# Kernel tuning notes

Measured on AMD Instinct MI355X. Metric: run time of the kernel, lower is better.

Reference implementation:

```python
import jax, jax.numpy as jnp
import numpy as np

B, N = 128, 196
HDIM, VDIM, ATT = 512, 2048, 512


def setup_inputs() -> dict:
    key = jax.random.key(0)
    ks = jax.random.split(key, 8)
    s_w = 1.0 / np.sqrt(HDIM)
    s_u = 1.0 / np.sqrt(VDIM)
    s_v = 1.0 / np.sqrt(ATT)
    return {
        "h": jax.random.normal(ks[0], (B, HDIM), dtype=jnp.float32),
        "V": jax.random.normal(ks[1], (B, N, VDIM), dtype=jnp.float32),
        "Ww": jax.random.uniform(ks[2], (HDIM, ATT), jnp.float32, -s_w, s_w),
        "Wb": jax.random.uniform(ks[3], (ATT,), jnp.float32, -s_w, s_w),
        "Uw": jax.random.uniform(ks[4], (VDIM, ATT), jnp.float32, -s_u, s_u),
        "Ub": jax.random.uniform(ks[5], (ATT,), jnp.float32, -s_u, s_u),
        "vw": jax.random.uniform(ks[6], (ATT, 1), jnp.float32, -s_v, s_v),
        "vb": jax.random.uniform(ks[7], (1,), jnp.float32, -s_v, s_v),
    }


def reference(h, V, Ww, Wb, Uw, Ub, vw, vb):
    # W(h): [B, A]; U(V): [B, N, A]
    wh = h @ Ww + Wb
    uv = jnp.einsum("bnv,va->bna", V, Uw) + Ub
    # e: [B, N, 1] scores via v(tanh(...))
    e = jnp.tanh(wh[:, None, :] + uv) @ vw + vb
    a = jax.nn.softmax(e, axis=1)          # softmax over N locations
    ctx = jnp.sum(a * V, axis=1)            # [B, vdim]
    return ctx, a.squeeze(-1)
```

## Files before the change

### kernel.cpp

```cpp
#include <hip/hip_runtime.h>
#include <hip/hip_bf16.h>

#define B_    128
#define N_    196
#define HDIM  512
#define VDIM  2048
#define ATT   512
#define M_TOT (B_ * N_)

#define BM  128
#define BKK 64
#define BN  128
#define NT  (VDIM / BKK)

typedef float  f32x4  __attribute__((ext_vector_type(4)));
typedef __bf16 bf16x8 __attribute__((ext_vector_type(8)));

__device__ __forceinline__ void gload_lds16(const void* g, void* l) {
    __builtin_amdgcn_global_load_lds(
        (const __attribute__((address_space(1))) void*)g,
        (__attribute__((address_space(3))) void*)l, 16, 0, 0);
}

__device__ __forceinline__ float fast_tanh(float x) {
    float ax = fabsf(x);
    float e  = __expf(-2.f * ax);
    float t  = (1.f - e) / (1.f + e);
    return copysignf(t, x);
}

__global__ void k_conv(const float* __restrict__ V, __bf16* __restrict__ Vb, int n8) {
    int idx    = blockIdx.x * blockDim.x + threadIdx.x;
    int stride = gridDim.x * blockDim.x;
    for (int i = idx; i < n8; i += stride) {
        const float4* s = reinterpret_cast<const float4*>(V + (size_t)i * 8);
        float4 x = s[0], y = s[1];
        bf16x8 w;
        w[0] = (__bf16)x.x; w[1] = (__bf16)x.y; w[2] = (__bf16)x.z; w[3] = (__bf16)x.w;
        w[4] = (__bf16)y.x; w[5] = (__bf16)y.y; w[6] = (__bf16)y.z; w[7] = (__bf16)y.w;
        reinterpret_cast<bf16x8*>(Vb)[i] = w;
    }
}

__global__ void k_transpose(const float* __restrict__ Uw, __bf16* __restrict__ UwT) {
    __shared__ __bf16 st[64][65];
    int k0 = blockIdx.x * 64;
    int c0 = blockIdx.y * 64;
    int t  = threadIdx.x;
#pragma unroll
    for (int i = 0; i < 16; ++i) {
        int lin = i * 256 + t;
        int kk = lin >> 6, cc = lin & 63;
        st[kk][cc] = (__bf16)Uw[(size_t)(k0 + kk) * ATT + c0 + cc];
    }
    __syncthreads();
#pragma unroll
    for (int i = 0; i < 16; ++i) {
        int lin = i * 256 + t;
        int cc = lin >> 6, kk = lin & 63;
        UwT[(size_t)(c0 + cc) * VDIM + k0 + kk] = st[kk][cc];
    }
}

__global__ void k_wh(const float* __restrict__ h, const float* __restrict__ Ww,
                     const float* __restrict__ Wb, const float* __restrict__ Ub,
                     float* __restrict__ whp) {
    __shared__ float hs[HDIM];
    int b = blockIdx.x;
    int t = threadIdx.x;
    hs[t]       = h[(size_t)b * HDIM + t];
    hs[t + 256] = h[(size_t)b * HDIM + t + 256];
    __syncthreads();
    float acc0 = 0.f, acc1 = 0.f;
    for (int k = 0; k < HDIM; ++k) {
        float hv = hs[k];
        acc0 += hv * Ww[(size_t)k * ATT + t];
        acc1 += hv * Ww[(size_t)k * ATT + t + 256];
    }
    whp[(size_t)b * ATT + t]       = acc0 + Wb[t] + Ub[t];
    whp[(size_t)b * ATT + t + 256] = acc1 + Wb[t + 256] + Ub[t + 256];
}

template <bool PRECONV>
__global__ __launch_bounds__(256, 2) void k_scores(
    const float* __restrict__ Vf, const __bf16* __restrict__ Vb,
    const __bf16* __restrict__ UwT, const float* __restrict__ whp,
    const float* __restrict__ vw, float* __restrict__ e_part)
{
    __shared__ __align__(16) __bf16 As[2][BM][BKK];
    __shared__ __align__(16) __bf16 Bs[2][BN][BKK];
    __shared__ float red[2][BM];

    int bid = blockIdx.x;
    int lid = (bid & 7) * (784 / 8) + (bid >> 3);
    int mtile = lid >> 2;
    int cc    = lid & 3;
    int m0 = mtile * BM;
    int c0 = cc * BN;
    int t    = threadIdx.x;
    int lane = t & 63;
    int wave = t >> 6;
    int wr = wave >> 1;
    int wc = wave & 1;

    f32x4 acc[4][4];
#pragma unroll
    for (int i = 0; i < 4; ++i)
#pragma unroll
        for (int j = 0; j < 4; ++j) acc[i][j] = (f32x4){0.f, 0.f, 0.f, 0.f};

    int lr  = lane >> 3;
    int csw = ((lane & 7) ^ (lr & 7)) * 8;
    const __bf16* AgS = PRECONV ? (Vb + (size_t)(m0 + wave * 32 + lr) * VDIM + csw) : nullptr;
    const __bf16* BgS = UwT + (size_t)(c0 + wave * 32 + lr) * VDIM + csw;
    __bf16* Al0 = &As[0][wave * 32 + lr][(lane & 7) * 8];
    __bf16* Bl0 = &Bs[0][wave * 32 + lr][(lane & 7) * 8];

    int ra = t >> 1;
    int ka = (t & 1) * 32;
    const float* Af = PRECONV ? nullptr : (Vf + (size_t)(m0 + ra) * VDIM + ka);

    int lcol = lane & 15;
    int lg4  = lane >> 4;

#define STAGE(buf, kt)                                                          \
    do {                                                                        \
        int kk0 = (kt) * BKK;                                                   \
        if (PRECONV) {                                                          \
            _Pragma("unroll")                                                   \
            for (int i = 0; i < 4; ++i) {                                       \
                gload_lds16(AgS + kk0 + (size_t)i * 8 * VDIM,                   \
                            Al0 + (buf) * (BM * BKK) + i * 8 * BKK);            \
                gload_lds16(BgS + kk0 + (size_t)i * 8 * VDIM,                   \
                            Bl0 + (buf) * (BN * BKK) + i * 8 * BKK);            \
            }                                                                   \
        } else {                                                                \
            _Pragma("unroll")                                                   \
            for (int i = 0; i < 4; ++i)                                         \
                gload_lds16(BgS + kk0 + (size_t)i * 8 * VDIM,                   \
                            Bl0 + (buf) * (BN * BKK) + i * 8 * BKK);            \
            const float4* src = reinterpret_cast<const float4*>(Af + kk0);      \
            _Pragma("unroll")                                                   \
            for (int i = 0; i < 4; ++i) {                                       \
                float4 x = src[2 * i];                                          \
                float4 y = src[2 * i + 1];                                      \
                bf16x8 w;                                                       \
                w[0] = (__bf16)x.x; w[1] = (__bf16)x.y;                         \
                w[2] = (__bf16)x.z; w[3] = (__bf16)x.w;                         \
                w[4] = (__bf16)y.x; w[5] = (__bf16)y.y;                         \
                w[6] = (__bf16)y.z; w[7] = (__bf16)y.w;                         \
                int ch = (((t & 1) * 4 + i) ^ (ra & 7)) * 8;                    \
                *reinterpret_cast<bf16x8*>(&As[buf][ra][ch]) = w;               \
            }                                                                   \
        }                                                                       \
    } while (0)

    int arow_base = wr * 64;
    int bcol_base = wc * 64;

    STAGE(0, 0);
    __syncthreads();

    for (int kt = 0; kt < NT; ++kt) {
        int buf = kt & 1;
        if (kt + 1 < NT) STAGE(buf ^ 1, kt + 1);

#pragma unroll
        for (int ks = 0; ks < 2; ++ks) {
            bf16x8 af[4], bfr[4];
#pragma unroll
            for (int i = 0; i < 4; ++i) {
                int row = arow_base + i * 16 + lcol;
                int ch  = ((ks * 4 + lg4) ^ (row & 7)) * 8;
                af[i] = *reinterpret_cast<const bf16x8*>(&As[buf][row][ch]);
            }
#pragma unroll
            for (int j = 0; j < 4; ++j) {
                int row = bcol_base + j * 16 + lcol;
                int ch  = ((ks * 4 + lg4) ^ (row & 7)) * 8;
                bfr[j] = *reinterpret_cast<const bf16x8*>(&Bs[buf][row][ch]);
            }
            __builtin_amdgcn_s_setprio(1);
#pragma unroll
            for (int i = 0; i < 4; ++i)
#pragma unroll
                for (int j = 0; j < 4; ++j)
                    acc[i][j] = __builtin_amdgcn_mfma_f32_16x16x32_bf16(af[i], bfr[j], acc[i][j], 0, 0, 0);
            __builtin_amdgcn_s_setprio(0);
        }
        __syncthreads();
    }
#undef STAGE

    int lrow4 = lg4 * 4;
    float rowsum[4][4];
#pragma unroll
    for (int i = 0; i < 4; ++i)
#pragma unroll
        for (int r = 0; r < 4; ++r) rowsum[i][r] = 0.f;

#pragma unroll
    for (int j = 0; j < 4; ++j) {
        int col = c0 + wc * 64 + j * 16 + lcol;
        float vwv = vw[col];
#pragma unroll
        for (int i = 0; i < 4; ++i) {
#pragma unroll
            for (int r = 0; r < 4; ++r) {
                int m = m0 + wr * 64 + i * 16 + lrow4 + r;
                int b = m / N_;
                float x = acc[i][j][r] + whp[(size_t)b * ATT + col];
                rowsum[i][r] += fast_tanh(x) * vwv;
            }
        }
    }
#pragma unroll
    for (int i = 0; i < 4; ++i) {
#pragma unroll
        for (int r = 0; r < 4; ++r) {
            float v = rowsum[i][r];
            v += __shfl_xor(v, 1);
            v += __shfl_xor(v, 2);
            v += __shfl_xor(v, 4);
            v += __shfl_xor(v, 8);
            if (lcol == 0)
                red[wc][wr * 64 + i * 16 + lrow4 + r] = v;
        }
    }
    __syncthreads();
    if (t < BM)
        e_part[(size_t)cc * M_TOT + m0 + t] = red[0][t] + red[1][t];
}

__global__ void k_softmax(const float* __restrict__ e_part, const float* __restrict__ vb,
                          float* __restrict__ a_out) {
    int b = blockIdx.x;
    int t = threadIdx.x;
    __shared__ float sm[256];
    float ev = 0.f;
    float e  = -1e30f;
    if (t < N_) {
        int m = b * N_ + t;
        ev = e_part[m] + e_part[M_TOT + m] + e_part[2 * M_TOT + m] + e_part[3 * M_TOT + m] + vb[0];
        e = ev;
    }
    sm[t] = e;
    __syncthreads();
    for (int s = 128; s > 0; s >>= 1) {
        if (t < s) sm[t] = fmaxf(sm[t], sm[t + s]);
        __syncthreads();
    }
    float mx = sm[0];
    __syncthreads();
    float ex = (t < N_) ? __expf(ev - mx) : 0.f;
    sm[t] = ex;
    __syncthreads();
    for (int s = 128; s > 0; s >>= 1) {
        if (t < s) sm[t] += sm[t + s];
        __syncthreads();
    }
    float inv = 1.f / sm[0];
    if (t < N_) a_out[(size_t)b * N_ + t] = ex * inv;
}

__global__ void k_ctx_bf(const __bf16* __restrict__ Vb, const float* __restrict__ a,
                         float* __restrict__ ctx) {
    int b  = blockIdx.x;
    int ch = blockIdx.y;
    int t  = threadIdx.x;
    __shared__ float as_[N_];
    for (int i = t; i < N_; i += 128) as_[i] = a[(size_t)b * N_ + i];
    __syncthreads();
    int col = ch * 1024 + t * 8;
    const __bf16* Vp = Vb + (size_t)b * N_ * VDIM + col;
    float av[8] = {0.f, 0.f, 0.f, 0.f, 0.f, 0.f, 0.f, 0.f};
    for (int n = 0; n < N_; ++n) {
        bf16x8 v = *reinterpret_cast<const bf16x8*>(Vp + (size_t)n * VDIM);
        float an = as_[n];
#pragma unroll
        for (int j = 0; j < 8; ++j) av[j] += an * (float)v[j];
    }
    f32x4 lo = {av[0], av[1], av[2], av[3]};
    f32x4 hi = {av[4], av[5], av[6], av[7]};
    f32x4* dst = reinterpret_cast<f32x4*>(ctx + (size_t)b * VDIM + col);
    dst[0] = lo;
    dst[1] = hi;
}

__global__ void k_ctx_f32(const float* __restrict__ V, const float* __restrict__ a,
                          float* __restrict__ ctx) {
    int b  = blockIdx.x;
    int ch = blockIdx.y;
    int t  = threadIdx.x;
    __shared__ float as_[N_];
    for (int i = t; i < N_; i += 128) as_[i] = a[(size_t)b * N_ + i];
    __syncthreads();
    int col = ch * 512 + t * 4;
    const f32x4* Vp = reinterpret_cast<const f32x4*>(V + (size_t)b * N_ * VDIM + col);
    f32x4 accv = {0.f, 0.f, 0.f, 0.f};
    for (int n = 0; n < N_; ++n)
        accv += as_[n] * Vp[(size_t)n * (VDIM / 4)];
    *reinterpret_cast<f32x4*>(ctx + (size_t)b * VDIM + col) = accv;
}

extern "C" void kernel_launch(void* const* d_in, const int* in_sizes, int n_in,
                              void* d_out, int out_size, void* d_ws, size_t ws_size,
                              hipStream_t stream) {
    const float* h  = (const float*)d_in[0];
    const float* V  = (const float*)d_in[1];
    const float* Ww = (const float*)d_in[2];
    const float* Wb = (const float*)d_in[3];
    const float* Uw = (const float*)d_in[4];
    const float* Ub = (const float*)d_in[5];
    const float* vw = (const float*)d_in[6];
    const float* vb = (const float*)d_in[7];

    float* out     = (float*)d_out;
    float* ctx_out = out;
    float* a_out   = out + (size_t)B_ * VDIM;

    const size_t vb_bytes = (size_t)B_ * N_ * VDIM * sizeof(__bf16);
    const size_t tail     = 2u * 1024 * 1024 + 256 * 1024 + (size_t)4 * M_TOT * 4 + 4096;
    bool preconv = ws_size >= vb_bytes + tail;

    char*   ws   = (char*)d_ws;
    __bf16* Vb   = (__bf16*)ws;
    char*   rest = ws + (preconv ? vb_bytes : 0);
    __bf16* UwT   = (__bf16*)rest;
    float*  whp   = (float*)(rest + 2u * 1024 * 1024);
    float*  e_prt = (float*)(rest + 2u * 1024 * 1024 + 256 * 1024);

    if (preconv) {
        int n8 = (B_ * N_ * VDIM) / 8;
        k_conv<<<2048, 256, 0, stream>>>(V, Vb, n8);
    }
    k_transpose<<<dim3(VDIM / 64, ATT / 64), 256, 0, stream>>>(Uw, UwT);
    k_wh<<<dim3(B_), 256, 0, stream>>>(h, Ww, Wb, Ub, whp);
    if (preconv)
        k_scores<true><<<dim3((M_TOT / BM) * (ATT / BN)), 256, 0, stream>>>(V, Vb, UwT, whp, vw, e_prt);
    else
        k_scores<false><<<dim3((M_TOT / BM) * (ATT / BN)), 256, 0, stream>>>(V, Vb, UwT, whp, vw, e_prt);
    k_softmax<<<dim3(B_), 256, 0, stream>>>(e_prt, vb, a_out);
    if (preconv)
        k_ctx_bf<<<dim3(B_, 2), 128, 0, stream>>>(Vb, a_out, ctx_out);
    else
        k_ctx_f32<<<dim3(B_, 4), 128, 0, stream>>>(V, a_out, ctx_out);
}
```

Baseline: 177.8 us.

## Fuse V bf16 conversion into scores GEMM and merge prep kernels

Removes the separate fp32-to-bf16 conversion pass over V: the scores GEMM now loads fp32 V tiles into registers, converts them and writes them to padded LDS (stride 72 instead of an XOR swizzle). The column-tile-0 blocks also write the bf16 copy of V to global memory for the later context kernel. Prefetch of the next A tile into registers is overlapped with the MFMA work, and the transpose and W(h) kernels are merged into one launch. The aim is to avoid one full read and write of V and some launch overhead, at the cost of each GEMM block reading fp32 A four times (once per column tile) and higher register pressure.

```diff
diff --git a/kernel.cpp b/kernel.cpp
--- a/kernel.cpp
+++ b/kernel.cpp
@@ -12,6 +12,7 @@
 #define BKK 64
 #define BN  128
 #define NT  (VDIM / BKK)
+#define LDA 72
 
 typedef float  f32x4  __attribute__((ext_vector_type(4)));
 typedef __bf16 bf16x8 __attribute__((ext_vector_type(8)));
@@ -29,65 +30,52 @@
     return copysignf(t, x);
 }
 
-__global__ void k_conv(const float* __restrict__ V, __bf16* __restrict__ Vb, int n8) {
-    int idx    = blockIdx.x * blockDim.x + threadIdx.x;
-    int stride = gridDim.x * blockDim.x;
-    for (int i = idx; i < n8; i += stride) {
-        const float4* s = reinterpret_cast<const float4*>(V + (size_t)i * 8);
-        float4 x = s[0], y = s[1];
-        bf16x8 w;
-        w[0] = (__bf16)x.x; w[1] = (__bf16)x.y; w[2] = (__bf16)x.z; w[3] = (__bf16)x.w;
-        w[4] = (__bf16)y.x; w[5] = (__bf16)y.y; w[6] = (__bf16)y.z; w[7] = (__bf16)y.w;
-        reinterpret_cast<bf16x8*>(Vb)[i] = w;
-    }
-}
-
-__global__ void k_transpose(const float* __restrict__ Uw, __bf16* __restrict__ UwT) {
-    __shared__ __bf16 st[64][65];
-    int k0 = blockIdx.x * 64;
-    int c0 = blockIdx.y * 64;
-    int t  = threadIdx.x;
-#pragma unroll
-    for (int i = 0; i < 16; ++i) {
-        int lin = i * 256 + t;
-        int kk = lin >> 6, cc = lin & 63;
-        st[kk][cc] = (__bf16)Uw[(size_t)(k0 + kk) * ATT + c0 + cc];
-    }
-    __syncthreads();
-#pragma unroll
-    for (int i = 0; i < 16; ++i) {
-        int lin = i * 256 + t;
-        int cc = lin >> 6, kk = lin & 63;
-        UwT[(size_t)(c0 + cc) * VDIM + k0 + kk] = st[kk][cc];
-    }
-}
-
-__global__ void k_wh(const float* __restrict__ h, const float* __restrict__ Ww,
-                     const float* __restrict__ Wb, const float* __restrict__ Ub,
-                     float* __restrict__ whp) {
-    __shared__ float hs[HDIM];
-    int b = blockIdx.x;
+__global__ void k_prep(const float* __restrict__ Uw, __bf16* __restrict__ UwT,
+                       const float* __restrict__ h, const float* __restrict__ Ww,
+                       const float* __restrict__ Wb, const float* __restrict__ Ub,
+                       float* __restrict__ whp) {
     int t = threadIdx.x;
-    hs[t]       = h[(size_t)b * HDIM + t];
-    hs[t + 256] = h[(size_t)b * HDIM + t + 256];
-    __syncthreads();
-    float acc0 = 0.f, acc1 = 0.f;
-    for (int k = 0; k < HDIM; ++k) {
-        float hv = hs[k];
-        acc0 += hv * Ww[(size_t)k * ATT + t];
-        acc1 += hv * Ww[(size_t)k * ATT + t + 256];
-    }
-    whp[(size_t)b * ATT + t]       = acc0 + Wb[t] + Ub[t];
-    whp[(size_t)b * ATT + t + 256] = acc1 + Wb[t + 256] + Ub[t + 256];
-}
-
-template <bool PRECONV>
+    if (blockIdx.x < 256) {
+        __shared__ __bf16 st[64][65];
+        int k0 = (blockIdx.x & 31) * 64;
+        int c0 = (blockIdx.x >> 5) * 64;
+#pragma unroll
+        for (int i = 0; i < 16; ++i) {
+            int lin = i * 256 + t;
+            int kk = lin >> 6, cc = lin & 63;
+            st[kk][cc] = (__bf16)Uw[(size_t)(k0 + kk) * ATT + c0 + cc];
+        }
+        __syncthreads();
+#pragma unroll
+        for (int i = 0; i < 16; ++i) {
+            int lin = i * 256 + t;
+            int cc = lin >> 6, kk = lin & 63;
+            UwT[(size_t)(c0 + cc) * VDIM + k0 + kk] = st[kk][cc];
+        }
+    } else {
+        __shared__ float hs[HDIM];
+        int b = blockIdx.x - 256;
+        hs[t]       = h[(size_t)b * HDIM + t];
+        hs[t + 256] = h[(size_t)b * HDIM + t + 256];
+        __syncthreads();
+        float acc0 = 0.f, acc1 = 0.f;
+        for (int k = 0; k < HDIM; ++k) {
+            float hv = hs[k];
+            acc0 += hv * Ww[(size_t)k * ATT + t];
+            acc1 += hv * Ww[(size_t)k * ATT + t + 256];
+        }
+        whp[(size_t)b * ATT + t]       = acc0 + Wb[t] + Ub[t];
+        whp[(size_t)b * ATT + t + 256] = acc1 + Wb[t + 256] + Ub[t + 256];
+    }
+}
+
+template <bool WRITE_VB>
 __global__ __launch_bounds__(256, 2) void k_scores(
-    const float* __restrict__ Vf, const __bf16* __restrict__ Vb,
+    const float* __restrict__ Vf, __bf16* __restrict__ Vb,
     const __bf16* __restrict__ UwT, const float* __restrict__ whp,
     const float* __restrict__ vw, float* __restrict__ e_part)
 {
-    __shared__ __align__(16) __bf16 As[2][BM][BKK];
+    __shared__ __align__(16) __bf16 As[2][BM][LDA];
     __shared__ __align__(16) __bf16 Bs[2][BN][BKK];
     __shared__ float red[2][BM];
 
@@ -111,68 +99,73 @@
 
     int lr  = lane >> 3;
     int csw = ((lane & 7) ^ (lr & 7)) * 8;
-    const __bf16* AgS = PRECONV ? (Vb + (size_t)(m0 + wave * 32 + lr) * VDIM + csw) : nullptr;
     const __bf16* BgS = UwT + (size_t)(c0 + wave * 32 + lr) * VDIM + csw;
-    __bf16* Al0 = &As[0][wave * 32 + lr][(lane & 7) * 8];
     __bf16* Bl0 = &Bs[0][wave * 32 + lr][(lane & 7) * 8];
 
     int ra = t >> 1;
     int ka = (t & 1) * 32;
-    const float* Af = PRECONV ? nullptr : (Vf + (size_t)(m0 + ra) * VDIM + ka);
+    const float*  Af  = Vf + (size_t)(m0 + ra) * VDIM + ka;
+    __bf16*       VbR = WRITE_VB ? (Vb + (size_t)(m0 + ra) * VDIM) : nullptr;
+    const bool    do_store = WRITE_VB && (cc == 0);
+
+    float4 aA[8];
+
+#define A_LOAD(kt)                                                              \
+    do {                                                                        \
+        const float4* src = reinterpret_cast<const float4*>(Af + (kt) * BKK);   \
+        _Pragma("unroll")                                                       \
+        for (int i = 0; i < 8; ++i) aA[i] = src[i];                             \
+    } while (0)
+
+#define B_GLOAD(buf, kt)                                                        \
+    do {                                                                        \
+        _Pragma("unroll")                                                       \
+        for (int i = 0; i < 4; ++i)                                             \
+            gload_lds16(BgS + (kt) * BKK + (size_t)i * 8 * VDIM,                \
+                        Bl0 + (buf) * (BN * BKK) + i * 8 * BKK);                \
+    } while (0)
+
+#define A_WRITE(buf, kt)                                                        \
+    do {                                                                        \
+        _Pragma("unroll")                                                       \
+        for (int i = 0; i < 4; ++i) {                                           \
+            float4 x = aA[2 * i], y = aA[2 * i + 1];                            \
+            bf16x8 w;                                                           \
+            w[0] = (__bf16)x.x; w[1] = (__bf16)x.y;                             \
+            w[2] = (__bf16)x.z; w[3] = (__bf16)x.w;                             \
+            w[4] = (__bf16)y.x; w[5] = (__bf16)y.y;                             \
+            w[6] = (__bf16)y.z; w[7] = (__bf16)y.w;                             \
+            int ch = (t & 1) * 4 + i;                                           \
+            *reinterpret_cast<bf16x8*>(&As[buf][ra][ch * 8]) = w;               \
+            if (do_store)                                                       \
+                *reinterpret_cast<bf16x8*>(VbR + (kt) * BKK + ch * 8) = w;      \
+        }                                                                       \
+    } while (0)
 
     int lcol = lane & 15;
     int lg4  = lane >> 4;
-
-#define STAGE(buf, kt)                                                          \
-    do {                                                                        \
-        int kk0 = (kt) * BKK;                                                   \
-        if (PRECONV) {                                                          \
-            _Pragma("unroll")                                                   \
-            for (int i = 0; i < 4; ++i) {                                       \
-                gload_lds16(AgS + kk0 + (size_t)i * 8 * VDIM,                   \
-                            Al0 + (buf) * (BM * BKK) + i * 8 * BKK);            \
-                gload_lds16(BgS + kk0 + (size_t)i * 8 * VDIM,                   \
-                            Bl0 + (buf) * (BN * BKK) + i * 8 * BKK);            \
-            }                                                                   \
-        } else {                                                                \
-            _Pragma("unroll")                                                   \
-            for (int i = 0; i < 4; ++i)                                         \
-                gload_lds16(BgS + kk0 + (size_t)i * 8 * VDIM,                   \
-                            Bl0 + (buf) * (BN * BKK) + i * 8 * BKK);            \
-            const float4* src = reinterpret_cast<const float4*>(Af + kk0);      \
-            _Pragma("unroll")                                                   \
-            for (int i = 0; i < 4; ++i) {                                       \
-                float4 x = src[2 * i];                                          \
-                float4 y = src[2 * i + 1];                                      \
-                bf16x8 w;                                                       \
-                w[0] = (__bf16)x.x; w[1] = (__bf16)x.y;                         \
-                w[2] = (__bf16)x.z; w[3] = (__bf16)x.w;                         \
-                w[4] = (__bf16)y.x; w[5] = (__bf16)y.y;                         \
-                w[6] = (__bf16)y.z; w[7] = (__bf16)y.w;                         \
-                int ch = (((t & 1) * 4 + i) ^ (ra & 7)) * 8;                    \
-                *reinterpret_cast<bf16x8*>(&As[buf][ra][ch]) = w;               \
-            }                                                                   \
-        }                                                                       \
-    } while (0)
-
     int arow_base = wr * 64;
     int bcol_base = wc * 64;
 
-    STAGE(0, 0);
+    A_LOAD(0);
+    B_GLOAD(0, 0);
+    A_WRITE(0, 0);
     __syncthreads();
 
     for (int kt = 0; kt < NT; ++kt) {
         int buf = kt & 1;
-        if (kt + 1 < NT) STAGE(buf ^ 1, kt + 1);
-
+        bool pf = (kt + 1 < NT);
+        if (pf) {
+            A_LOAD(kt + 1);
+            B_GLOAD(buf ^ 1, kt + 1);
+        }
 #pragma unroll
         for (int ks = 0; ks < 2; ++ks) {
             bf16x8 af[4], bfr[4];
 #pragma unroll
             for (int i = 0; i < 4; ++i) {
                 int row = arow_base + i * 16 + lcol;
-                int ch  = ((ks * 4 + lg4) ^ (row & 7)) * 8;
-                af[i] = *reinterpret_cast<const bf16x8*>(&As[buf][row][ch]);
+                af[i] = *reinterpret_cast<const bf16x8*>(&As[buf][row][ks * 32 + lg4 * 8]);
             }
 #pragma unroll
             for (int j = 0; j < 4; ++j) {
@@ -188,9 +181,12 @@
                     acc[i][j] = __builtin_amdgcn_mfma_f32_16x16x32_bf16(af[i], bfr[j], acc[i][j], 0, 0, 0);
             __builtin_amdgcn_s_setprio(0);
         }
-        __syncthreads();
-    }
-#undef STAGE
+        if (pf) A_WRITE(buf ^ 1, kt + 1);
+        __syncthreads();
+    }
+#undef A_LOAD
+#undef B_GLOAD
+#undef A_WRITE
 
     int lrow4 = lg4 * 4;
     float rowsum[4][4];
@@ -321,27 +317,22 @@
 
     const size_t vb_bytes = (size_t)B_ * N_ * VDIM * sizeof(__bf16);
     const size_t tail     = 2u * 1024 * 1024 + 256 * 1024 + (size_t)4 * M_TOT * 4 + 4096;
-    bool preconv = ws_size >= vb_bytes + tail;
+    bool write_vb = ws_size >= vb_bytes + tail;
 
     char*   ws   = (char*)d_ws;
     __bf16* Vb   = (__bf16*)ws;
-    char*   rest = ws + (preconv ? vb_bytes : 0);
+    char*   rest = ws + (write_vb ? vb_bytes : 0);
     __bf16* UwT   = (__bf16*)rest;
     float*  whp   = (float*)(rest + 2u * 1024 * 1024);
     float*  e_prt = (float*)(rest + 2u * 1024 * 1024 + 256 * 1024);
 
-    if (preconv) {
-        int n8 = (B_ * N_ * VDIM) / 8;
-        k_conv<<<2048, 256, 0, stream>>>(V, Vb, n8);
-    }
-    k_transpose<<<dim3(VDIM / 64, ATT / 64), 256, 0, stream>>>(Uw, UwT);
-    k_wh<<<dim3(B_), 256, 0, stream>>>(h, Ww, Wb, Ub, whp);
-    if (preconv)
-        k_scores<true><<<dim3((M_TOT / BM) * (ATT / BN)), 256, 0, stream>>>(V, Vb, UwT, whp, vw, e_prt);
+    k_prep<<<dim3(384), 256, 0, stream>>>(Uw, UwT, h, Ww, Wb, Ub, whp);
+    if (write_vb)
+        k_scores<true><<<dim3(784), 256, 0, stream>>>(V, Vb, UwT, whp, vw, e_prt);
     else
-        k_scores<false><<<dim3((M_TOT / BM) * (ATT / BN)), 256, 0, stream>>>(V, Vb, UwT, whp, vw, e_prt);
+        k_scores<false><<<dim3(784), 256, 0, stream>>>(V, Vb, UwT, whp, vw, e_prt);
     k_softmax<<<dim3(B_), 256, 0, stream>>>(e_prt, vb, a_out);
-    if (preconv)
+    if (write_vb)
         k_ctx_bf<<<dim3(B_, 2), 128, 0, stream>>>(Vb, a_out, ctx_out);
     else
         k_ctx_f32<<<dim3(B_, 4), 128, 0, stream>>>(V, a_out, ctx_out);
```

Result: slower. 304.2 us (+71.1%).
